# Optimization experiments

Hardware: AMD Instinct MI355X
Metric: run time of the kernel (lower is better)

Reference implementation:

```python
import jax, jax.numpy as jnp
import numpy as np

NUM_SLOTS = 8
ITERS = 3
EPS = 1e-8
LN_EPS = 1e-5
B, N, D = 64, 4096, 128
H = 256


def _ln(x, w, b):
    m = jnp.mean(x, axis=-1, keepdims=True)
    v = jnp.mean(jnp.square(x - m), axis=-1, keepdims=True)
    return (x - m) * jax.lax.rsqrt(v + LN_EPS) * w + b


def setup_inputs() -> dict:
    key = jax.random.key(0)
    ks = jax.random.split(key, 10)
    s = 0.02
    return {
        "inputs": jax.random.normal(ks[0], (B, N, D), jnp.float32),
        "noise": jax.random.normal(ks[1], (B, NUM_SLOTS, D), jnp.float32),
        "ln_in_w": jnp.ones((D,), jnp.float32), "ln_in_b": jnp.zeros((D,), jnp.float32),
        "ln_s_w": jnp.ones((D,), jnp.float32), "ln_s_b": jnp.zeros((D,), jnp.float32),
        "ln_m_w": jnp.ones((D,), jnp.float32), "ln_m_b": jnp.zeros((D,), jnp.float32),
        "slot_mu": jnp.zeros((1, 1, D), jnp.float32),
        "slot_sigma": jnp.ones((1, 1, D), jnp.float32),
        "Wq": s * jax.random.normal(ks[2], (D, D), jnp.float32),
        "Wk": s * jax.random.normal(ks[3], (D, D), jnp.float32),
        "Wv": s * jax.random.normal(ks[4], (D, D), jnp.float32),
        "W_ih": s * jax.random.normal(ks[5], (3 * D, D), jnp.float32),
        "W_hh": s * jax.random.normal(ks[6], (3 * D, D), jnp.float32),
        "b_ih": jnp.zeros((3 * D,), jnp.float32), "b_hh": jnp.zeros((3 * D,), jnp.float32),
        "W1": s * jax.random.normal(ks[7], (H, D), jnp.float32), "b1": jnp.zeros((H,), jnp.float32),
        "W2": s * jax.random.normal(ks[8], (D, H), jnp.float32), "b2": jnp.zeros((D,), jnp.float32),
    }


def reference(inputs, noise, ln_in_w, ln_in_b, ln_s_w, ln_s_b, ln_m_w, ln_m_b,
              slot_mu, slot_sigma, Wq, Wk, Wv, W_ih, W_hh, b_ih, b_hh, W1, b1, W2, b2):
    b, n, d = inputs.shape
    x = _ln(inputs, ln_in_w, ln_in_b)
    sigma = jax.nn.softplus(slot_sigma)
    slots = slot_mu + sigma * noise  # [b, S, d]
    k = jnp.einsum('bnd,ed->bne', x, Wk)
    v = jnp.einsum('bnd,ed->bne', x, Wv)
    scale = 1.0 / jnp.sqrt(jnp.asarray(d, inputs.dtype))
    for _ in range(ITERS):
        slots_prev = slots
        q = jnp.einsum('bsd,ed->bse', _ln(slots, ln_s_w, ln_s_b), Wq)
        dots = jnp.einsum('bne,bse->bns', k, q) * scale  # [b, n, S]
        attn = jax.nn.softmax(dots, axis=-1) + EPS       # softmax over slots
        attn = attn / jnp.sum(attn, axis=-2, keepdims=True)  # normalize over inputs
        updates = jnp.einsum('bns,bnd->bsd', attn, v)
        # GRUCell: input=updates, hidden=slots_prev
        gi = jnp.einsum('bsd,ed->bse', updates, W_ih) + b_ih      # [b,S,3d]
        gh = jnp.einsum('bsd,ed->bse', slots_prev, W_hh) + b_hh
        i_r, i_z, i_n = jnp.split(gi, 3, axis=-1)
        h_r, h_z, h_n = jnp.split(gh, 3, axis=-1)
        r = jax.nn.sigmoid(i_r + h_r)
        z = jax.nn.sigmoid(i_z + h_z)
        nn_ = jnp.tanh(i_n + r * h_n)
        slots = (1.0 - z) * nn_ + z * slots_prev
    h = jax.nn.relu(jnp.einsum('bsd,hd->bsh', _ln(slots, ln_m_w, ln_m_b), W1) + b1)
    slots = slots + jnp.einsum('bsh,dh->bsd', h, W2) + b2
    return slots
```

## Files before the change

kernel.cpp:

```cpp
#include <hip/hip_runtime.h>
#include <math.h>

#define NB 64
#define NN 4096
#define ND 128
#define NS 8
#define NH 256
#define CHUNKS 16
#define ROWS_PER_CHUNK 256

static constexpr float EPSA  = 1e-8f;
static constexpr float LNE   = 1e-5f;
static constexpr float SCALE = 0.08838834764831845f;

#define OFF_SLOTS 0
#define OFF_QK    65536
#define OFF_WC    131072
#define OFF_M2T   180224
#define OFF_QKB   196608
#define OFF_UPD   196736
#define OFF_CS    262272
#define OFF_PART  262784
#define OFF_PCS   1311360

__device__ __forceinline__ float dot4f(float4 a, float4 b) {
    return fmaf(a.x, b.x, fmaf(a.y, b.y, fmaf(a.z, b.z, a.w * b.w)));
}

template <int CTRL>
__device__ __forceinline__ float dpp_radd(float v) {
    return v + __int_as_float(__builtin_amdgcn_update_dpp(
        __float_as_int(v), __float_as_int(v), CTRL, 0xF, 0xF, false));
}
__device__ __forceinline__ float red16(float v) {
    v = dpp_radd<0xB1>(v); v = dpp_radd<0x4E>(v);
    v = dpp_radd<0x141>(v); v = dpp_radd<0x140>(v);
    return v;
}
__device__ __forceinline__ float red8(float v) {
    v = dpp_radd<0xB1>(v); v = dpp_radd<0x4E>(v); v = dpp_radd<0x141>(v);
    return v;
}

__global__ __launch_bounds__(256) void prep_kernel(
    const float* __restrict__ noise, const float* __restrict__ ln_s_w,
    const float* __restrict__ ln_s_b, const float* __restrict__ slot_mu,
    const float* __restrict__ slot_sigma, const float* __restrict__ Wq,
    const float* __restrict__ Wk, const float* __restrict__ Wv,
    const float* __restrict__ W_ih, float* __restrict__ ws)
{
    int bid = blockIdx.x, t = threadIdx.x;
    if (bid < 32) {
        int i0 = (bid * 256 + t) * 8;
        int d0 = i0 & 127;
        float o[8];
#pragma unroll
        for (int j = 0; j < 8; j++) {
            float sg = slot_sigma[d0 + j];
            float sp = fmaxf(sg, 0.f) + log1pf(expf(-fabsf(sg)));
            o[j] = fmaf(sp, noise[i0 + j], slot_mu[d0 + j]);
        }
        float4* dst = (float4*)(ws + OFF_SLOTS + i0);
        dst[0] = make_float4(o[0], o[1], o[2], o[3]);
        dst[1] = make_float4(o[4], o[5], o[6], o[7]);
    } else if (bid < 224) {
        int g = (bid - 32) * 2 + (t >> 7);
        int f = t & 127;
        const float* wih = W_ih + g * ND;
        float acc = 0.f;
        for (int e = 0; e < ND; e++) acc = fmaf(wih[e], Wv[e * ND + f], acc);
        ws[OFF_WC + g * ND + f] = acc;
    } else {
        int dp = (bid - 224) * 2 + (t >> 7);
        int d = t & 127;
        float acc = 0.f;
        for (int e = 0; e < ND; e++) acc = fmaf(Wq[e * ND + d], Wk[e * ND + dp], acc);
        ws[OFF_M2T + dp * ND + d] = SCALE * ln_s_w[d] * acc;
        float c = ln_s_b[d] * acc;
#pragma unroll
        for (int m = 1; m <= 32; m <<= 1) c += __shfl_xor(c, m, 64);
        __shared__ float red[4];
        if ((t & 63) == 0) red[t >> 6] = c;
        __syncthreads();
        if (t == 0)   ws[OFF_QKB + dp] = SCALE * (red[0] + red[1]);
        if (t == 128) ws[OFF_QKB + dp] = SCALE * (red[2] + red[3]);
    }
}

__global__ __launch_bounds__(512) void qk0_kernel(float* __restrict__ ws)
{
    __shared__ float sh_s[NS * ND];
    __shared__ float sh_ln[NS * ND];
    int b = blockIdx.x, t = threadIdx.x;
    sh_s[t]       = ws[OFF_SLOTS + b * NS * ND + t];
    sh_s[t + 512] = ws[OFF_SLOTS + b * NS * ND + t + 512];
    __syncthreads();
    {
        int wid = t >> 6, l = t & 63;
        float v0 = sh_s[wid * ND + 2 * l], v1 = sh_s[wid * ND + 2 * l + 1];
        float s1 = v0 + v1, s2 = fmaf(v0, v0, v1 * v1);
#pragma unroll
        for (int m = 1; m <= 32; m <<= 1) { s1 += __shfl_xor(s1, m, 64); s2 += __shfl_xor(s2, m, 64); }
        float mean = s1 * (1.f / 128.f);
        float var = fmaf(-mean, mean, s2 * (1.f / 128.f));
        float tv = var + LNE;
        float rs = rsqrtf(tv); rs = rs * (1.5f - 0.5f * tv * rs * rs);
        sh_ln[wid * ND + 2 * l]     = (v0 - mean) * rs;
        sh_ln[wid * ND + 2 * l + 1] = (v1 - mean) * rs;
    }
    __syncthreads();
    {
        int g = t >> 3, c = t & 7, s = g >> 3, dp0 = g & 7;
        const float4* lp = (const float4*)(sh_ln + s * ND + c * 16);
        float4 l0 = lp[0], l1 = lp[1], l2 = lp[2], l3 = lp[3];
#pragma unroll 2
        for (int j = 0; j < 16; j++) {
            int dp = dp0 + 8 * j;
            const float4* m4 = (const float4*)(ws + OFF_M2T + dp * ND + c * 16);
            float a = dot4f(m4[0], l0) + dot4f(m4[1], l1) + dot4f(m4[2], l2) + dot4f(m4[3], l3);
            a = red8(a);
            if (c == 0) ws[OFF_QK + b * NS * ND + s * ND + dp] = a + ws[OFF_QKB + dp];
        }
    }
}

__global__ __launch_bounds__(256) void attn_kernel(
    const float* __restrict__ inp, const float* __restrict__ lnw,
    const float* __restrict__ lnb, float* __restrict__ ws)
{
    __shared__ float qk_lds[NS * ND];
    __shared__ float red_lds[4][NS][ND];
    __shared__ float cs_lds[4][NS];
    int t = threadIdx.x;
    int b = blockIdx.x >> 4, chunk = blockIdx.x & 15;
    int w = t >> 6, lane = t & 63;
    int rg = lane >> 4, colg = lane & 15;

    {
        const float4* src = (const float4*)(ws + OFF_QK + b * NS * ND);
        ((float4*)qk_lds)[t] = src[t];
    }
    float wv[8], bv[8];
    {
        const float4* w4 = (const float4*)(lnw + colg * 8);
        const float4* b4 = (const float4*)(lnb + colg * 8);
        float4 wa = w4[0], wb = w4[1], ba = b4[0], bb = b4[1];
        wv[0]=wa.x; wv[1]=wa.y; wv[2]=wa.z; wv[3]=wa.w; wv[4]=wb.x; wv[5]=wb.y; wv[6]=wb.z; wv[7]=wb.w;
        bv[0]=ba.x; bv[1]=ba.y; bv[2]=ba.z; bv[3]=ba.w; bv[4]=bb.x; bv[5]=bb.y; bv[6]=bb.z; bv[7]=bb.w;
    }
    float acc[NS][8];
    float cs[NS];
#pragma unroll
    for (int si = 0; si < NS; si++) {
        cs[si] = 0.f;
#pragma unroll
        for (int j = 0; j < 8; j++) acc[si][j] = 0.f;
    }
    __syncthreads();

    const float* base = inp + ((size_t)b * NN + chunk * ROWS_PER_CHUNK + w * 64 + rg) * ND + colg * 8;
#pragma unroll 2
    for (int q = 0; q < 16; q++) {
        const float* rp = base + q * 4 * ND;
        float4 a0 = *(const float4*)rp;
        float4 a1 = *(const float4*)(rp + 4);
        float x[8] = {a0.x, a0.y, a0.z, a0.w, a1.x, a1.y, a1.z, a1.w};
        float s1 = 0.f, s2 = 0.f;
#pragma unroll
        for (int j = 0; j < 8; j++) { s1 += x[j]; s2 = fmaf(x[j], x[j], s2); }
        s1 = red16(s1); s2 = red16(s2);
        float mean = s1 * (1.f / 128.f);
        float var = fmaf(-mean, mean, s2 * (1.f / 128.f));
        float tv = var + LNE;
        float rs = rsqrtf(tv); rs = rs * (1.5f - 0.5f * tv * rs * rs);
#pragma unroll
        for (int j = 0; j < 8; j++) x[j] = fmaf((x[j] - mean) * rs, wv[j], bv[j]);

        float pd[NS];
#pragma unroll
        for (int si = 0; si < NS; si++) {
            const float4* q4 = (const float4*)(qk_lds + si * ND + colg * 8);
            float4 q0 = q4[0], q1 = q4[1];
            float p = x[0] * q0.x;
            p = fmaf(x[1], q0.y, p); p = fmaf(x[2], q0.z, p); p = fmaf(x[3], q0.w, p);
            p = fmaf(x[4], q1.x, p); p = fmaf(x[5], q1.y, p); p = fmaf(x[6], q1.z, p);
            p = fmaf(x[7], q1.w, p);
            pd[si] = red16(p);
        }
        float mx = fmaxf(fmaxf(fmaxf(pd[0], pd[1]), fmaxf(pd[2], pd[3])),
                         fmaxf(fmaxf(pd[4], pd[5]), fmaxf(pd[6], pd[7])));
        float ev[NS]; float es = 0.f;
#pragma unroll
        for (int si = 0; si < NS; si++) { ev[si] = __expf(pd[si] - mx); es += ev[si]; }
        float r0 = __builtin_amdgcn_rcpf(es);
        float inv = r0 * (2.0f - es * r0);
#pragma unroll
        for (int si = 0; si < NS; si++) {
            float p = ev[si] * inv;
            cs[si] += p;
#pragma unroll
            for (int j = 0; j < 8; j++) acc[si][j] = fmaf(p, x[j], acc[si][j]);
        }
    }
#pragma unroll
    for (int m = 16; m <= 32; m <<= 1) {
#pragma unroll
        for (int si = 0; si < NS; si++) {
            cs[si] += __shfl_xor(cs[si], m, 64);
#pragma unroll
            for (int j = 0; j < 8; j++) acc[si][j] += __shfl_xor(acc[si][j], m, 64);
        }
    }
    if (lane < 16) {
#pragma unroll
        for (int si = 0; si < NS; si++) {
            *(float4*)&red_lds[w][si][lane * 8]     = make_float4(acc[si][0], acc[si][1], acc[si][2], acc[si][3]);
            *(float4*)&red_lds[w][si][lane * 8 + 4] = make_float4(acc[si][4], acc[si][5], acc[si][6], acc[si][7]);
        }
    }
    if (lane == 0) {
#pragma unroll
        for (int si = 0; si < NS; si++) cs_lds[w][si] = cs[si];
    }
    __syncthreads();
    float* pout = ws + OFF_PART + (size_t)(b * CHUNKS + chunk) * (NS * ND);
#pragma unroll
    for (int k = 0; k < 4; k++) {
        int o = t + k * 256;
        pout[o] = red_lds[0][0][o] + red_lds[1][0][o] + red_lds[2][0][o] + red_lds[3][0][o];
    }
    if (t < NS) {
        ws[OFF_PCS + (b * CHUNKS + chunk) * NS + t] =
            cs_lds[0][t] + cs_lds[1][t] + cs_lds[2][t] + cs_lds[3][t];
    }
}

__global__ __launch_bounds__(128) void reduce_kernel(float* __restrict__ ws)
{
    int b = blockIdx.x >> 3, s = blockIdx.x & 7, t = threadIdx.x;
    const float* part = ws + OFF_PART + (size_t)b * CHUNKS * NS * ND + s * ND;
    float r = 0.f;
#pragma unroll
    for (int p = 0; p < CHUNKS; p++) r += part[p * (NS * ND) + t];
    ws[OFF_UPD + (b * NS + s) * ND + t] = r;
    if (t < 16) {
        float c = ws[OFF_PCS + (b * CHUNKS + t) * NS + s];
        c = red16(c);
        if (t == 0) ws[OFF_CS + b * NS + s] = c;
    }
}

template <int LAST>
__global__ __launch_bounds__(512) void gru_kernel(
    const float* __restrict__ W_hh, const float* __restrict__ b_ih,
    const float* __restrict__ b_hh, const float* __restrict__ W1,
    const float* __restrict__ b1, const float* __restrict__ W2,
    const float* __restrict__ b2, const float* __restrict__ ln_m_w,
    const float* __restrict__ ln_m_b, float* __restrict__ ws,
    float* __restrict__ out)
{
    __shared__ float sh_nr[4 * ND];
    __shared__ float sh_sp[4 * ND];
    __shared__ float sh_sx[ND];
    __shared__ float sh_cs[4];
    __shared__ float sh_gi[4 * 384];
    __shared__ float sh_gh[4 * 384];
    __shared__ float sh_ln[4 * ND];
    int b = blockIdx.x >> 1, sh2 = blockIdx.x & 1;
    int t = threadIdx.x;

    float r = ws[OFF_UPD + b * NS * ND + sh2 * 512 + t];
    sh_sp[t] = ws[OFF_SLOTS + b * NS * ND + sh2 * 512 + t];
    if (t < ND) {
        float a = 0.f;
#pragma unroll
        for (int s = 0; s < NS; s++) a += ws[OFF_UPD + b * NS * ND + s * ND + t];
        sh_sx[t] = a;
    }
    if (t < 4) sh_cs[t] = ws[OFF_CS + b * NS + sh2 * 4 + t] + (float)NN * EPSA;
    __syncthreads();
    sh_nr[t] = fmaf(EPSA, sh_sx[t & 127], r) / sh_cs[t >> 7];
    __syncthreads();
    int g = t >> 3, c = t & 7;
    int sl = g >> 4, g3 = g & 15;
    {
        const float4* np = (const float4*)(sh_nr + sl * ND + c * 16);
        const float4* pp = (const float4*)(sh_sp + sl * ND + c * 16);
        float4 n0 = np[0], n1 = np[1], n2 = np[2], n3 = np[3];
        float4 p0 = pp[0], p1 = pp[1], p2 = pp[2], p3 = pp[3];
#pragma unroll 4
        for (int j = 0; j < 24; j++) {
            int e3 = g3 + 16 * j;
            const float4* wc4 = (const float4*)(ws + OFF_WC + e3 * ND + c * 16);
            const float4* wh4 = (const float4*)(W_hh + e3 * ND + c * 16);
            float ai = dot4f(wc4[0], n0) + dot4f(wc4[1], n1) + dot4f(wc4[2], n2) + dot4f(wc4[3], n3);
            float ah = dot4f(wh4[0], p0) + dot4f(wh4[1], p1) + dot4f(wh4[2], p2) + dot4f(wh4[3], p3);
            ai = red8(ai); ah = red8(ah);
            if (c == 0) {
                sh_gi[sl * 384 + e3] = ai + b_ih[e3];
                sh_gh[sl * 384 + e3] = ah + b_hh[e3];
            }
        }
    }
    __syncthreads();
    {
        int si = t >> 7, d = t & 127;
        float gir = sh_gi[si * 384 + d],       ghr = sh_gh[si * 384 + d];
        float giz = sh_gi[si * 384 + 128 + d], ghz = sh_gh[si * 384 + 128 + d];
        float gin = sh_gi[si * 384 + 256 + d], ghn = sh_gh[si * 384 + 256 + d];
        float rr = 1.f / (1.f + expf(-(gir + ghr)));
        float z  = 1.f / (1.f + expf(-(giz + ghz)));
        float nn_ = tanhf(fmaf(rr, ghn, gin));
        float ns = fmaf(z, sh_sp[t] - nn_, nn_);
        sh_nr[t] = ns;
        if (!LAST) ws[OFF_SLOTS + b * NS * ND + sh2 * 512 + t] = ns;
    }
    __syncthreads();
    {
        int wid = t >> 6, l = t & 63;
        if (wid < 4) {
            float v0 = sh_nr[wid * ND + 2 * l], v1 = sh_nr[wid * ND + 2 * l + 1];
            float s1 = v0 + v1, s2 = fmaf(v0, v0, v1 * v1);
#pragma unroll
            for (int m = 1; m <= 32; m <<= 1) { s1 += __shfl_xor(s1, m, 64); s2 += __shfl_xor(s2, m, 64); }
            float mean = s1 * (1.f / 128.f);
            float var = fmaf(-mean, mean, s2 * (1.f / 128.f));
            float tv = var + LNE;
            float rs = rsqrtf(tv); rs = rs * (1.5f - 0.5f * tv * rs * rs);
            float x0 = (v0 - mean) * rs, x1 = (v1 - mean) * rs;
            if (LAST) {
                x0 = fmaf(x0, ln_m_w[2 * l],     ln_m_b[2 * l]);
                x1 = fmaf(x1, ln_m_w[2 * l + 1], ln_m_b[2 * l + 1]);
            }
            sh_ln[wid * ND + 2 * l]     = x0;
            sh_ln[wid * ND + 2 * l + 1] = x1;
        }
    }
    __syncthreads();
    if (!LAST) {
        const float4* lp = (const float4*)(sh_ln + sl * ND + c * 16);
        float4 l0 = lp[0], l1 = lp[1], l2 = lp[2], l3 = lp[3];
#pragma unroll 2
        for (int j = 0; j < 8; j++) {
            int dp = g3 + 16 * j;
            const float4* m4 = (const float4*)(ws + OFF_M2T + dp * ND + c * 16);
            float a = dot4f(m4[0], l0) + dot4f(m4[1], l1) + dot4f(m4[2], l2) + dot4f(m4[3], l3);
            a = red8(a);
            if (c == 0) ws[OFF_QK + b * NS * ND + (sh2 * 4 + sl) * ND + dp] = a + ws[OFF_QKB + dp];
        }
    } else {
        const float4* lp = (const float4*)(sh_ln + sl * ND + c * 16);
        float4 l0 = lp[0], l1 = lp[1], l2 = lp[2], l3 = lp[3];
#pragma unroll 2
        for (int j = 0; j < 16; j++) {
            int hh = g3 + 16 * j;
            const float4* w14 = (const float4*)(W1 + hh * ND + c * 16);
            float a = dot4f(w14[0], l0) + dot4f(w14[1], l1) + dot4f(w14[2], l2) + dot4f(w14[3], l3);
            a = red8(a);
            if (c == 0) sh_gi[sl * NH + hh] = fmaxf(a + b1[hh], 0.f);
        }
        __syncthreads();
        const float4* hp = (const float4*)(sh_gi + sl * NH + c * 32);
        float4 h0 = hp[0], h1 = hp[1], h2 = hp[2], h3 = hp[3];
        float4 h4 = hp[4], h5 = hp[5], h6 = hp[6], h7 = hp[7];
#pragma unroll 2
        for (int j = 0; j < 8; j++) {
            int d = g3 + 16 * j;
            const float4* w24 = (const float4*)(W2 + d * NH + c * 32);
            float a = dot4f(w24[0], h0) + dot4f(w24[1], h1) + dot4f(w24[2], h2) + dot4f(w24[3], h3)
                    + dot4f(w24[4], h4) + dot4f(w24[5], h5) + dot4f(w24[6], h6) + dot4f(w24[7], h7);
            a = red8(a);
            if (c == 0) out[(size_t)b * NS * ND + (sh2 * 4 + sl) * ND + d] = a + b2[d] + sh_nr[sl * ND + d];
        }
    }
}

extern "C" void kernel_launch(void* const* d_in, const int* in_sizes, int n_in,
                              void* d_out, int out_size, void* d_ws, size_t ws_size,
                              hipStream_t stream) {
    (void)in_sizes; (void)n_in; (void)out_size; (void)ws_size;
    const float* inputs     = (const float*)d_in[0];
    const float* noise      = (const float*)d_in[1];
    const float* ln_in_w    = (const float*)d_in[2];
    const float* ln_in_b    = (const float*)d_in[3];
    const float* ln_s_w     = (const float*)d_in[4];
    const float* ln_s_b     = (const float*)d_in[5];
    const float* ln_m_w     = (const float*)d_in[6];
    const float* ln_m_b     = (const float*)d_in[7];
    const float* slot_mu    = (const float*)d_in[8];
    const float* slot_sigma = (const float*)d_in[9];
    const float* Wq         = (const float*)d_in[10];
    const float* Wk         = (const float*)d_in[11];
    const float* Wv         = (const float*)d_in[12];
    const float* W_ih       = (const float*)d_in[13];
    const float* W_hh       = (const float*)d_in[14];
    const float* b_ih       = (const float*)d_in[15];
    const float* b_hh       = (const float*)d_in[16];
    const float* W1         = (const float*)d_in[17];
    const float* b1         = (const float*)d_in[18];
    const float* W2         = (const float*)d_in[19];
    const float* b2         = (const float*)d_in[20];
    float* ws  = (float*)d_ws;
    float* out = (float*)d_out;

    hipLaunchKernelGGL(prep_kernel, dim3(288), dim3(256), 0, stream,
                       noise, ln_s_w, ln_s_b, slot_mu, slot_sigma, Wq, Wk, Wv, W_ih, ws);
    hipLaunchKernelGGL(qk0_kernel, dim3(NB), dim3(512), 0, stream, ws);
    for (int it = 0; it < 3; ++it) {
        hipLaunchKernelGGL(attn_kernel, dim3(NB * CHUNKS), dim3(256), 0, stream,
                           inputs, ln_in_w, ln_in_b, ws);
        hipLaunchKernelGGL(reduce_kernel, dim3(NB * NS), dim3(128), 0, stream, ws);
        if (it < 2) {
            hipLaunchKernelGGL((gru_kernel<0>), dim3(NB * 2), dim3(512), 0, stream,
                               W_hh, b_ih, b_hh, W1, b1, W2, b2, ln_m_w, ln_m_b, ws, out);
        } else {
            hipLaunchKernelGGL((gru_kernel<1>), dim3(NB * 2), dim3(512), 0, stream,
                               W_hh, b_ih, b_hh, W1, b1, W2, b2, ln_m_w, ln_m_b, ws, out);
        }
    }
}
```

Measured before the change: 465.4 us.

## Fold layernorm affine into query weights, fuse chunk reduction into GRU kernel

Measured after the change: 485.6 us. 1.04x slower.

```diff
diff --git a/kernel.cpp b/kernel.cpp
--- a/kernel.cpp
+++ b/kernel.cpp
@@ -6,22 +6,22 @@
 #define ND 128
 #define NS 8
 #define NH 256
-#define CHUNKS 16
-#define ROWS_PER_CHUNK 256
+#define CHUNKS 8
+#define ROWS_PER_CHUNK 512
 
 static constexpr float EPSA  = 1e-8f;
 static constexpr float LNE   = 1e-5f;
 static constexpr float SCALE = 0.08838834764831845f;
+static constexpr float LOG2E = 1.4426950408889634f;
 
 #define OFF_SLOTS 0
 #define OFF_QK    65536
 #define OFF_WC    131072
 #define OFF_M2T   180224
 #define OFF_QKB   196608
-#define OFF_UPD   196736
-#define OFF_CS    262272
-#define OFF_PART  262784
-#define OFF_PCS   1311360
+#define OFF_PA1   196736
+#define OFF_PA2   721024
+#define OFF_PA3   725120
 
 __device__ __forceinline__ float dot4f(float4 a, float4 b) {
     return fmaf(a.x, b.x, fmaf(a.y, b.y, fmaf(a.z, b.z, a.w * b.w)));
@@ -128,39 +128,51 @@
     const float* __restrict__ inp, const float* __restrict__ lnw,
     const float* __restrict__ lnb, float* __restrict__ ws)
 {
-    __shared__ float qk_lds[NS * ND];
     __shared__ float red_lds[4][NS][ND];
-    __shared__ float cs_lds[4][NS];
+    __shared__ float cs2_lds[4][NS];
+    __shared__ float cs3_lds[4][NS];
     int t = threadIdx.x;
-    int b = blockIdx.x >> 4, chunk = blockIdx.x & 15;
+    int b = blockIdx.x >> 3, chunk = blockIdx.x & 7;
     int w = t >> 6, lane = t & 63;
     int rg = lane >> 4, colg = lane & 15;
 
-    {
-        const float4* src = (const float4*)(ws + OFF_QK + b * NS * ND);
-        ((float4*)qk_lds)[t] = src[t];
-    }
-    float wv[8], bv[8];
-    {
+    float qk2[NS][8];
+    float S1[NS], B2[NS];
+    {
+        float wv[8], bv[8];
         const float4* w4 = (const float4*)(lnw + colg * 8);
         const float4* b4 = (const float4*)(lnb + colg * 8);
         float4 wa = w4[0], wb = w4[1], ba = b4[0], bb = b4[1];
         wv[0]=wa.x; wv[1]=wa.y; wv[2]=wa.z; wv[3]=wa.w; wv[4]=wb.x; wv[5]=wb.y; wv[6]=wb.z; wv[7]=wb.w;
         bv[0]=ba.x; bv[1]=ba.y; bv[2]=ba.z; bv[3]=ba.w; bv[4]=bb.x; bv[5]=bb.y; bv[6]=bb.z; bv[7]=bb.w;
-    }
-    float acc[NS][8];
-    float cs[NS];
+        const float* qkp = ws + OFF_QK + b * NS * ND;
+#pragma unroll
+        for (int si = 0; si < NS; si++) {
+            const float4* qr = (const float4*)(qkp + si * ND + colg * 8);
+            float4 q0 = qr[0], q1 = qr[1];
+            float q8[8] = {q0.x, q0.y, q0.z, q0.w, q1.x, q1.y, q1.z, q1.w};
+            float ss = 0.f, bb2 = 0.f;
+#pragma unroll
+            for (int j = 0; j < 8; j++) {
+                float v = LOG2E * wv[j] * q8[j];
+                qk2[si][j] = v;
+                ss += v;
+                bb2 = fmaf(bv[j], q8[j], bb2);
+            }
+            S1[si] = red16(ss);
+            B2[si] = LOG2E * red16(bb2);
+        }
+    }
+    float acc1[NS][8], acc2[NS], acc3[NS];
 #pragma unroll
     for (int si = 0; si < NS; si++) {
-        cs[si] = 0.f;
-#pragma unroll
-        for (int j = 0; j < 8; j++) acc[si][j] = 0.f;
-    }
-    __syncthreads();
-
-    const float* base = inp + ((size_t)b * NN + chunk * ROWS_PER_CHUNK + w * 64 + rg) * ND + colg * 8;
-#pragma unroll 2
-    for (int q = 0; q < 16; q++) {
+        acc2[si] = 0.f; acc3[si] = 0.f;
+#pragma unroll
+        for (int j = 0; j < 8; j++) acc1[si][j] = 0.f;
+    }
+
+    const float* base = inp + ((size_t)b * NN + chunk * ROWS_PER_CHUNK + w * 128 + rg) * ND + colg * 8;
+    for (int q = 0; q < 32; q++) {
         const float* rp = base + q * 4 * ND;
         float4 a0 = *(const float4*)rp;
         float4 a1 = *(const float4*)(rp + 4);
@@ -173,85 +185,75 @@
         float var = fmaf(-mean, mean, s2 * (1.f / 128.f));
         float tv = var + LNE;
         float rs = rsqrtf(tv); rs = rs * (1.5f - 0.5f * tv * rs * rs);
-#pragma unroll
-        for (int j = 0; j < 8; j++) x[j] = fmaf((x[j] - mean) * rs, wv[j], bv[j]);
-
         float pd[NS];
 #pragma unroll
         for (int si = 0; si < NS; si++) {
-            const float4* q4 = (const float4*)(qk_lds + si * ND + colg * 8);
-            float4 q0 = q4[0], q1 = q4[1];
-            float p = x[0] * q0.x;
-            p = fmaf(x[1], q0.y, p); p = fmaf(x[2], q0.z, p); p = fmaf(x[3], q0.w, p);
-            p = fmaf(x[4], q1.x, p); p = fmaf(x[5], q1.y, p); p = fmaf(x[6], q1.z, p);
-            p = fmaf(x[7], q1.w, p);
+            float p = x[0] * qk2[si][0];
+#pragma unroll
+            for (int j = 1; j < 8; j++) p = fmaf(x[j], qk2[si][j], p);
             pd[si] = red16(p);
         }
+        float rm = rs * mean;
+#pragma unroll
+        for (int si = 0; si < NS; si++)
+            pd[si] = fmaf(rs, pd[si], fmaf(-rm, S1[si], B2[si]));
         float mx = fmaxf(fmaxf(fmaxf(pd[0], pd[1]), fmaxf(pd[2], pd[3])),
                          fmaxf(fmaxf(pd[4], pd[5]), fmaxf(pd[6], pd[7])));
         float ev[NS]; float es = 0.f;
 #pragma unroll
-        for (int si = 0; si < NS; si++) { ev[si] = __expf(pd[si] - mx); es += ev[si]; }
+        for (int si = 0; si < NS; si++) { ev[si] = exp2f(pd[si] - mx); es += ev[si]; }
         float r0 = __builtin_amdgcn_rcpf(es);
         float inv = r0 * (2.0f - es * r0);
+        float invrs = inv * rs;
 #pragma unroll
         for (int si = 0; si < NS; si++) {
-            float p = ev[si] * inv;
-            cs[si] += p;
-#pragma unroll
-            for (int j = 0; j < 8; j++) acc[si][j] = fmaf(p, x[j], acc[si][j]);
+            float pr = ev[si] * invrs;
+            float pn = ev[si] * inv;
+            acc3[si] += pn;
+            acc2[si] = fmaf(pr, mean, acc2[si]);
+#pragma unroll
+            for (int j = 0; j < 8; j++) acc1[si][j] = fmaf(pr, x[j], acc1[si][j]);
         }
     }
 #pragma unroll
     for (int m = 16; m <= 32; m <<= 1) {
 #pragma unroll
         for (int si = 0; si < NS; si++) {
-            cs[si] += __shfl_xor(cs[si], m, 64);
-#pragma unroll
-            for (int j = 0; j < 8; j++) acc[si][j] += __shfl_xor(acc[si][j], m, 64);
+            acc2[si] += __shfl_xor(acc2[si], m, 64);
+            acc3[si] += __shfl_xor(acc3[si], m, 64);
+#pragma unroll
+            for (int j = 0; j < 8; j++) acc1[si][j] += __shfl_xor(acc1[si][j], m, 64);
         }
     }
     if (lane < 16) {
 #pragma unroll
         for (int si = 0; si < NS; si++) {
-            *(float4*)&red_lds[w][si][lane * 8]     = make_float4(acc[si][0], acc[si][1], acc[si][2], acc[si][3]);
-            *(float4*)&red_lds[w][si][lane * 8 + 4] = make_float4(acc[si][4], acc[si][5], acc[si][6], acc[si][7]);
+            *(float4*)&red_lds[w][si][lane * 8]     = make_float4(acc1[si][0], acc1[si][1], acc1[si][2], acc1[si][3]);
+            *(float4*)&red_lds[w][si][lane * 8 + 4] = make_float4(acc1[si][4], acc1[si][5], acc1[si][6], acc1[si][7]);
         }
     }
     if (lane == 0) {
 #pragma unroll
-        for (int si = 0; si < NS; si++) cs_lds[w][si] = cs[si];
-    }
-    __syncthreads();
-    float* pout = ws + OFF_PART + (size_t)(b * CHUNKS + chunk) * (NS * ND);
+        for (int si = 0; si < NS; si++) { cs2_lds[w][si] = acc2[si]; cs3_lds[w][si] = acc3[si]; }
+    }
+    __syncthreads();
+    float* p1 = ws + OFF_PA1 + (size_t)(b * CHUNKS + chunk) * (NS * ND);
 #pragma unroll
     for (int k = 0; k < 4; k++) {
         int o = t + k * 256;
-        pout[o] = red_lds[0][0][o] + red_lds[1][0][o] + red_lds[2][0][o] + red_lds[3][0][o];
+        p1[o] = red_lds[0][0][o] + red_lds[1][0][o] + red_lds[2][0][o] + red_lds[3][0][o];
     }
     if (t < NS) {
-        ws[OFF_PCS + (b * CHUNKS + chunk) * NS + t] =
-            cs_lds[0][t] + cs_lds[1][t] + cs_lds[2][t] + cs_lds[3][t];
-    }
-}
-
-__global__ __launch_bounds__(128) void reduce_kernel(float* __restrict__ ws)
-{
-    int b = blockIdx.x >> 3, s = blockIdx.x & 7, t = threadIdx.x;
-    const float* part = ws + OFF_PART + (size_t)b * CHUNKS * NS * ND + s * ND;
-    float r = 0.f;
-#pragma unroll
-    for (int p = 0; p < CHUNKS; p++) r += part[p * (NS * ND) + t];
-    ws[OFF_UPD + (b * NS + s) * ND + t] = r;
-    if (t < 16) {
-        float c = ws[OFF_PCS + (b * CHUNKS + t) * NS + s];
-        c = red16(c);
-        if (t == 0) ws[OFF_CS + b * NS + s] = c;
+        ws[OFF_PA2 + (b * CHUNKS + chunk) * NS + t] =
+            cs2_lds[0][t] + cs2_lds[1][t] + cs2_lds[2][t] + cs2_lds[3][t];
+        ws[OFF_PA3 + (b * CHUNKS + chunk) * NS + t] =
+            cs3_lds[0][t] + cs3_lds[1][t] + cs3_lds[2][t] + cs3_lds[3][t];
     }
 }
 
 template <int LAST>
 __global__ __launch_bounds__(512) void gru_kernel(
+    const float* __restrict__ lnw, const float* __restrict__ lnb,
     const float* __restrict__ W_hh, const float* __restrict__ b_ih,
     const float* __restrict__ b_hh, const float* __restrict__ W1,
     const float* __restrict__ b1, const float* __restrict__ W2,
@@ -261,25 +263,57 @@
 {
     __shared__ float sh_nr[4 * ND];
     __shared__ float sh_sp[4 * ND];
+    __shared__ float sh_tmp[512];
     __shared__ float sh_sx[ND];
-    __shared__ float sh_cs[4];
+    __shared__ float sh_a2[NS];
+    __shared__ float sh_a3[NS];
     __shared__ float sh_gi[4 * 384];
     __shared__ float sh_gh[4 * 384];
     __shared__ float sh_ln[4 * ND];
     int b = blockIdx.x >> 1, sh2 = blockIdx.x & 1;
     int t = threadIdx.x;
-
-    float r = ws[OFF_UPD + b * NS * ND + sh2 * 512 + t];
+    int e = t & 127;
+
+    const float* pa1 = ws + OFF_PA1 + (size_t)b * CHUNKS * NS * ND;
+    float r1 = 0.f;
+#pragma unroll
+    for (int p = 0; p < CHUNKS; p++) r1 += pa1[p * (NS * ND) + sh2 * 512 + t];
+    {
+        int sg = t >> 7;
+        float ax = 0.f;
+#pragma unroll
+        for (int p = 0; p < CHUNKS; p++)
+            ax += pa1[p * (NS * ND) + sg * ND + e] + pa1[p * (NS * ND) + (sg + 4) * ND + e];
+        sh_tmp[t] = ax;
+    }
+    if (t < NS) {
+        float a = 0.f;
+#pragma unroll
+        for (int p = 0; p < CHUNKS; p++) a += ws[OFF_PA2 + (b * CHUNKS + p) * NS + t];
+        sh_a2[t] = a;
+    }
+    if (t >= 64 && t < 64 + NS) {
+        float a = 0.f;
+#pragma unroll
+        for (int p = 0; p < CHUNKS; p++) a += ws[OFF_PA3 + (b * CHUNKS + p) * NS + (t - 64)];
+        sh_a3[t - 64] = a;
+    }
     sh_sp[t] = ws[OFF_SLOTS + b * NS * ND + sh2 * 512 + t];
-    if (t < ND) {
-        float a = 0.f;
-#pragma unroll
-        for (int s = 0; s < NS; s++) a += ws[OFF_UPD + b * NS * ND + s * ND + t];
-        sh_sx[t] = a;
-    }
-    if (t < 4) sh_cs[t] = ws[OFF_CS + b * NS + sh2 * 4 + t] + (float)NN * EPSA;
-    __syncthreads();
-    sh_nr[t] = fmaf(EPSA, sh_sx[t & 127], r) / sh_cs[t >> 7];
+    __syncthreads();
+    if (t < ND) sh_sx[t] = sh_tmp[t] + sh_tmp[t + 128] + sh_tmp[t + 256] + sh_tmp[t + 384];
+    __syncthreads();
+    {
+        int sl_ = t >> 7;
+        int s = sh2 * 4 + sl_;
+        float we = lnw[e], be = lnb[e];
+        float a2s = sh_a2[s], a3s = sh_a3[s];
+        float A2sum = 0.f, A3sum = 0.f;
+#pragma unroll
+        for (int k = 0; k < NS; k++) { A2sum += sh_a2[k]; A3sum += sh_a3[k]; }
+        float Sx = fmaf(we, sh_sx[e] - A2sum, be * A3sum);
+        float raw = fmaf(we, r1 - a2s, be * a3s);
+        sh_nr[t] = (raw + EPSA * Sx) / (a3s + (float)NN * EPSA);
+    }
     __syncthreads();
     int g = t >> 3, c = t & 7;
     int sl = g >> 4, g3 = g & 15;
@@ -409,13 +443,14 @@
     for (int it = 0; it < 3; ++it) {
         hipLaunchKernelGGL(attn_kernel, dim3(NB * CHUNKS), dim3(256), 0, stream,
                            inputs, ln_in_w, ln_in_b, ws);
-        hipLaunchKernelGGL(reduce_kernel, dim3(NB * NS), dim3(128), 0, stream, ws);
         if (it < 2) {
             hipLaunchKernelGGL((gru_kernel<0>), dim3(NB * 2), dim3(512), 0, stream,
-                               W_hh, b_ih, b_hh, W1, b1, W2, b2, ln_m_w, ln_m_b, ws, out);
+                               ln_in_w, ln_in_b, W_hh, b_ih, b_hh, W1, b1, W2, b2,
+                               ln_m_w, ln_m_b, ws, out);
         } else {
             hipLaunchKernelGGL((gru_kernel<1>), dim3(NB * 2), dim3(512), 0, stream,
-                               W_hh, b_ih, b_hh, W1, b1, W2, b2, ln_m_w, ln_m_b, ws, out);
-        }
-    }
-}
+                               ln_in_w, ln_in_b, W_hh, b_ih, b_hh, W1, b1, W2, b2,
+                               ln_m_w, ln_m_b, ws, out);
+        }
+    }
+}
```
